# Kernel optimization log

Hardware: AMD Instinct MI355X
Metric: run time of the kernel (lower is better)

## Reference

```python
import jax, jax.numpy as jnp
import numpy as np

C = 64
SIZE = 448
PATCH = 14
P2 = PATCH * PATCH                 # 196, per-chunk token count
SPLIT = (SIZE * SIZE) // P2        # 1024 chunks
TG = PATCH * 4                     # 56, pooled global resolution
POOL = SIZE // TG                  # 8, exact avg-pool factor
EPS = 1e-5


def setup_inputs() -> dict:
    key = jax.random.key(0)
    ks = jax.random.split(key, 10)
    b = 2
    x = jax.random.normal(ks[0], (b, C, SIZE, SIZE), dtype=jnp.float32)
    s = 1.0 / np.sqrt(C)
    return {
        "x": x,
        "gn_w": jnp.ones((C,), jnp.float32),
        "gn_b": jnp.zeros((C,), jnp.float32),
        "q_w": jax.random.normal(ks[1], (C, C), jnp.float32) * s,
        "q_b": jnp.zeros((C,), jnp.float32),
        "k_w": jax.random.normal(ks[2], (C, C), jnp.float32) * s,
        "k_b": jnp.zeros((C,), jnp.float32),
        "v_w": jax.random.normal(ks[3], (C, C), jnp.float32) * s,
        "v_b": jnp.zeros((C,), jnp.float32),
        "proj_w": jax.random.normal(ks[4], (C, C), jnp.float32) * s,
    }


def _conv1x1(t, W, bias=None):
    out = jnp.einsum('oc,bchw->bohw', W, t)
    if bias is not None:
        out = out + bias[None, :, None, None]
    return out


def _group_norm(x, w, b):
    # GroupNorm(num_groups=1): normalize over (C,H,W) per sample
    mean = x.mean(axis=(1, 2, 3), keepdims=True)
    var = x.var(axis=(1, 2, 3), keepdims=True)
    xn = (x - mean) * jax.lax.rsqrt(var + EPS)
    return xn * w[None, :, None, None] + b[None, :, None, None]


def reference(x, gn_w, gn_b, q_w, q_b, k_w, k_b, v_w, v_b, proj_w):
    b, c, h, w = x.shape
    xn = _group_norm(x, gn_w, gn_b)
    q = _conv1x1(xn, q_w, q_b)
    k = _conv1x1(xn, k_w, k_b)
    v = _conv1x1(xn, v_w, v_b)

    # ---- patch-local attention (channels*chunks as feature dim S) ----
    S = c * SPLIT  # 65536
    qf = q.reshape(b, S, P2)
    kf = k.reshape(b, S, P2)
    vf = v.reshape(b, S, P2)
    wm = jnp.einsum('bsp,bsq->bpq', qf, kf) * (S ** -0.5)  # [b,196,196]
    wm = jax.nn.softmax(wm, axis=2)
    # h[b,s,q'] = sum_k v[b,s,k] * wm[b,q',k]
    hp = jnp.einsum('bsk,bqk->bsq', vf, wm).reshape(b, c, h, w)

    # ---- global pooled attention ----
    pool = lambda t: t.reshape(b, c, TG, POOL, TG, POOL).mean(axis=(3, 5))
    qg = pool(q).reshape(b, c, TG * TG)
    kg = pool(k).reshape(b, c, TG * TG)
    vg = pool(v).reshape(b, c, TG * TG)
    wg = jnp.einsum('bcp,bcq->bpq', qg, kg) * (c ** -0.5)  # [b,3136,3136]
    wg = jax.nn.softmax(wg, axis=2)
    hg = jnp.einsum('bck,bqk->bcq', vg, wg).reshape(b, c, TG, TG)
    hg = jnp.repeat(jnp.repeat(hg, POOL, axis=2), POOL, axis=3)

    h_in = 0.75 * hp + 0.25 * hg
    out = _conv1x1(h_in, proj_w)  # proj_out, no bias
    return x + out
```

## Files before the change

kernel.cpp:

```cpp
#include <hip/hip_runtime.h>

#define NB 2
#define NC 64
#define HW 200704
#define CHW 12845056
#define P2 196
#define NCHUNK 1024
#define NCELL 3136
#define WMN 38416

typedef __attribute__((ext_vector_type(8))) short bfrag;
typedef __attribute__((ext_vector_type(4))) float ffrag;
typedef __attribute__((ext_vector_type(4))) short short4v;
typedef __attribute__((ext_vector_type(4))) float float4v;

#define MFMA16(A,B,C) __builtin_amdgcn_mfma_f32_16x16x32_bf16(A,B,C,0,0,0)

__device__ __forceinline__ short f2bf(float f) {
  unsigned u = __builtin_bit_cast(unsigned, f);
  u = u + 0x7FFFu + ((u >> 16) & 1u);
  return (short)(u >> 16);
}

__global__ __launch_bounds__(64) void k1_stats_pool(
    const float* __restrict__ x, float* __restrict__ xpool, float* __restrict__ partials) {
  int bx = blockIdx.x;
  int batch = bx / (64*56);
  int c = (bx / 56) % 64;
  int pr = bx % 56;
  int l = threadIdx.x;
  const float* xp = x + (size_t)batch*CHW + (size_t)c*HW + pr*8*448;
  float cell = 0.f, s2 = 0.f;
  if (l < 56) {
    #pragma unroll
    for (int r = 0; r < 8; ++r) {
      float4v a = *(const float4v*)(xp + r*448 + l*8);
      float4v b = *(const float4v*)(xp + r*448 + l*8 + 4);
      #pragma unroll
      for (int j = 0; j < 4; ++j) { cell += a[j] + b[j]; s2 += a[j]*a[j] + b[j]*b[j]; }
    }
    xpool[((size_t)batch*64 + c)*NCELL + pr*56 + l] = cell * (1.f/64.f);
  }
  float s1 = (l < 56) ? cell : 0.f;
  #pragma unroll
  for (int m = 1; m < 64; m <<= 1) { s1 += __shfl_xor(s1, m, 64); s2 += __shfl_xor(s2, m, 64); }
  if (l == 0) { partials[bx*2] = s1; partials[bx*2 + 1] = s2; }
}

__global__ __launch_bounds__(256) void k1b_reduce(
    const float* __restrict__ partials, float* __restrict__ stats) {
  __shared__ float red[2][256];
  int t = threadIdx.x;
  for (int b = 0; b < NB; ++b) {
    float s1 = 0.f, s2 = 0.f;
    for (int i = t; i < 3584; i += 256) {
      s1 += partials[(b*3584 + i)*2];
      s2 += partials[(b*3584 + i)*2 + 1];
    }
    red[0][t] = s1; red[1][t] = s2;
    __syncthreads();
    for (int m = 128; m > 0; m >>= 1) {
      if (t < m) { red[0][t] += red[0][t+m]; red[1][t] += red[1][t+m]; }
      __syncthreads();
    }
    if (t == 0) { stats[b*2] = red[0][0]; stats[b*2+1] = red[1][0]; }
    __syncthreads();
  }
}

__global__ __launch_bounds__(256) void k2_qkv(
    const float* __restrict__ x, const float* __restrict__ gnw, const float* __restrict__ gnb,
    const float* __restrict__ qw, const float* __restrict__ qb,
    const float* __restrict__ kw, const float* __restrict__ kb,
    const float* __restrict__ vw, const float* __restrict__ vb,
    const float* __restrict__ stats,
    short* __restrict__ qx, short* __restrict__ kx, short* __restrict__ vnat) {
  __shared__ __attribute__((aligned(16))) short xnt[256*72];
  int bx = blockIdx.x;
  int batch = bx / 784;
  int px0 = (bx % 784) * 256;
  int t = threadIdx.x;
  float s1 = stats[batch*2], s2 = stats[batch*2+1];
  float mean = s1 * (1.f/CHW);
  float rstd = rsqrtf(s2*(1.f/CHW) - mean*mean + 1e-5f);
  for (int it = 0; it < 64; it += 4) {
    float vv[4];
    #pragma unroll
    for (int r = 0; r < 4; ++r) {
      float v = x[(size_t)batch*CHW + (size_t)(it+r)*HW + px0 + t];
      vv[r] = (v - mean) * rstd * gnw[it+r] + gnb[it+r];
    }
    short4v s;
    #pragma unroll
    for (int r = 0; r < 4; ++r) s[r] = f2bf(vv[r]);
    *(short4v*)(xnt + t*72 + it) = s;
  }
  __syncthreads();
  int l = t & 63, w = t >> 6, li = l & 15, q_ = l >> 4;
  bfrag bfr[4][2];
  #pragma unroll
  for (int nn = 0; nn < 4; ++nn) {
    int row = (w*4 + nn)*16 + li;
    bfr[nn][0] = *(const bfrag*)(xnt + row*72 + q_*8);
    bfr[nn][1] = *(const bfrag*)(xnt + row*72 + 32 + q_*8);
  }
  const float* Ws[3] = {qw, kw, vw};
  const float* Bs[3] = {qb, kb, vb};
  for (int T = 0; T < 3; ++T) {
    ffrag acc[4][4];
    #pragma unroll
    for (int mt = 0; mt < 4; ++mt) {
      bfrag a0, a1;
      const float* wp = Ws[T] + (mt*16 + li)*64;
      #pragma unroll
      for (int j = 0; j < 8; ++j) { a0[j] = f2bf(wp[q_*8 + j]); a1[j] = f2bf(wp[32 + q_*8 + j]); }
      #pragma unroll
      for (int nn = 0; nn < 4; ++nn) {
        ffrag z = {0.f,0.f,0.f,0.f};
        z = MFMA16(a0, bfr[nn][0], z);
        z = MFMA16(a1, bfr[nn][1], z);
        acc[mt][nn] = z;
      }
    }
    if (T < 2) {
      short* dstb = (T == 0 ? qx : kx) + (size_t)batch*HW*64;
      #pragma unroll
      for (int nn = 0; nn < 4; ++nn) {
        int px = px0 + (w*4 + nn)*16 + li;
        #pragma unroll
        for (int mt = 0; mt < 4; ++mt) {
          float4v bias = *(const float4v*)(Bs[T] + mt*16 + q_*4);
          short4v s;
          #pragma unroll
          for (int r = 0; r < 4; ++r) s[r] = f2bf(acc[mt][nn][r] + bias[r]);
          *(short4v*)(dstb + (size_t)px*64 + mt*16 + q_*4) = s;
        }
      }
    } else {
      #pragma unroll
      for (int nn = 0; nn < 4; ++nn) {
        int px = px0 + (w*4 + nn)*16 + li;
        #pragma unroll
        for (int mt = 0; mt < 4; ++mt) {
          float4v bias = *(const float4v*)(Bs[T] + mt*16 + q_*4);
          #pragma unroll
          for (int r = 0; r < 4; ++r) {
            int c = mt*16 + q_*4 + r;
            vnat[((size_t)batch*64 + c)*HW + px] = f2bf(acc[mt][nn][r] + bias[r]);
          }
        }
      }
    }
  }
}

__global__ __launch_bounds__(256) void k2a_pool_qkv(
    const float* __restrict__ xpool, const float* __restrict__ stats,
    const float* __restrict__ gnw, const float* __restrict__ gnb,
    const float* __restrict__ qw, const float* __restrict__ qb,
    const float* __restrict__ kw, const float* __restrict__ kb,
    const float* __restrict__ vw, const float* __restrict__ vb,
    short* __restrict__ qgt, short* __restrict__ kgt, short* __restrict__ vgn) {
  __shared__ float xs[64][64];
  int bx = blockIdx.x;
  int batch = bx / 49;
  int j0 = (bx % 49) * 64;
  int t = threadIdx.x;
  float s1 = stats[batch*2], s2 = stats[batch*2+1];
  float mean = s1 * (1.f/CHW);
  float rstd = rsqrtf(s2*(1.f/CHW) - mean*mean + 1e-5f);
  #pragma unroll
  for (int it = 0; it < 16; ++it) {
    int idx = t + it*256;
    int c = idx >> 6, jl = idx & 63;
    float v = xpool[((size_t)batch*64 + c)*NCELL + j0 + jl];
    xs[c][jl] = (v - mean)*rstd*gnw[c] + gnb[c];
  }
  __syncthreads();
  int jl = t & 63;
  int og = (t >> 6) * 16;
  int j = j0 + jl;
  for (int T = 0; T < 3; ++T) {
    const float* W  = (T==0 ? qw : (T==1 ? kw : vw));
    const float* Bv = (T==0 ? qb : (T==1 ? kb : vb));
    float o16[16];
    #pragma unroll
    for (int oo = 0; oo < 16; ++oo) o16[oo] = Bv[og+oo];
    for (int c = 0; c < 64; ++c) {
      float xv = xs[c][jl];
      #pragma unroll
      for (int oo = 0; oo < 16; ++oo) o16[oo] += W[(og+oo)*64 + c] * xv;
    }
    if (T < 2) {
      short* dst = (T==0 ? qgt : kgt) + ((size_t)batch*NCELL + j)*64 + og;
      #pragma unroll
      for (int oo = 0; oo < 16; oo += 4) {
        short4v s;
        #pragma unroll
        for (int r = 0; r < 4; ++r) s[r] = f2bf(o16[oo+r]);
        *(short4v*)(dst + oo) = s;
      }
    } else {
      #pragma unroll
      for (int oo = 0; oo < 16; ++oo)
        vgn[((size_t)batch*64 + og + oo)*NCELL + j] = f2bf(o16[oo]);
    }
  }
}

__global__ __launch_bounds__(512) void k3_wm(
    const short* __restrict__ qx, const short* __restrict__ kx, float* __restrict__ wmacc) {
  int bx = blockIdx.x;
  int batch = bx >> 6;
  int slab = bx & 63;
  int t = threadIdx.x;
  int l = t & 63, w = t >> 6, li = l & 15, q_ = l >> 4;
  int wm_ = w >> 2, wn = w & 3;
  int m0 = wm_ * 7, mcnt = wm_ ? 6 : 7;
  int nt0 = wn ? 4 + (wn-1)*3 : 0, ncnt = wn ? 3 : 4;
  ffrag acc[7][4];
  #pragma unroll
  for (int i = 0; i < 7; ++i)
    #pragma unroll
    for (int j = 0; j < 4; ++j) acc[i][j] = (ffrag){0.f,0.f,0.f,0.f};
  const short* qbase = qx + (size_t)batch*HW*64;
  const short* kbase = kx + (size_t)batch*HW*64;
  for (int c8 = 0; c8 < 16; ++c8) {
    int chunk = slab*16 + c8;
    const short* qc = qbase + (size_t)chunk*P2*64;
    const short* kc = kbase + (size_t)chunk*P2*64;
    #pragma unroll
    for (int ks = 0; ks < 2; ++ks) {
      int koff = ks*32 + q_*8;
      bfrag af[7], bf[4];
      #pragma unroll
      for (int mi = 0; mi < 7; ++mi) if (mi < mcnt)
        af[mi] = *(const bfrag*)(qc + (size_t)((m0+mi)*16 + li)*64 + koff);
      #pragma unroll
      for (int ni = 0; ni < 4; ++ni) if (ni < ncnt)
        bf[ni] = *(const bfrag*)(kc + (size_t)((nt0+ni)*16 + li)*64 + koff);
      #pragma unroll
      for (int mi = 0; mi < 7; ++mi) if (mi < mcnt)
        #pragma unroll
        for (int ni = 0; ni < 4; ++ni) if (ni < ncnt)
          acc[mi][ni] = MFMA16(af[mi], bf[ni], acc[mi][ni]);
    }
  }
  float* wdst = wmacc + (size_t)batch*WMN;
  #pragma unroll
  for (int mi = 0; mi < 7; ++mi) if (mi < mcnt)
    #pragma unroll
    for (int ni = 0; ni < 4; ++ni) if (ni < ncnt) {
      int qcol = (nt0+ni)*16 + li;
      if (qcol < 196)
        #pragma unroll
        for (int r = 0; r < 4; ++r) {
          int prow = (m0+mi)*16 + q_*4 + r;
          if (prow < 196) atomicAdd(wdst + prow*196 + qcol, acc[mi][ni][r]);
        }
    }
}

__global__ __launch_bounds__(64) void k4_softmax(
    const float* __restrict__ wmacc, short* __restrict__ P) {
  int bx = blockIdx.x;
  int batch = bx / 208;
  int p = bx % 208;
  int l = threadIdx.x;
  short* prow = P + ((size_t)batch*208 + p)*224;
  if (p >= 196) { for (int j = l; j < 224; j += 64) prow[j] = 0; return; }
  const float* src = wmacc + (size_t)batch*WMN + p*196;
  float v[4]; float mx = -1e30f;
  #pragma unroll
  for (int i = 0; i < 4; ++i) {
    int q = l + i*64;
    v[i] = (q < 196) ? src[q]*(1.f/256.f) : -1e30f;
    mx = fmaxf(mx, v[i]);
  }
  #pragma unroll
  for (int m = 1; m < 64; m <<= 1) mx = fmaxf(mx, __shfl_xor(mx, m, 64));
  float s = 0.f;
  #pragma unroll
  for (int i = 0; i < 4; ++i) { v[i] = __expf(v[i] - mx); s += v[i]; }
  #pragma unroll
  for (int m = 1; m < 64; m <<= 1) s += __shfl_xor(s, m, 64);
  float inv = 1.f / s;
  #pragma unroll
  for (int i = 0; i < 4; ++i) {
    int q = l + i*64;
    if (q < 224) prow[q] = (q < 196) ? f2bf(v[i]*inv) : (short)0;
  }
}

__global__ __launch_bounds__(256) void k5_gattn(
    const short* __restrict__ qgt, const short* __restrict__ kgt,
    const short* __restrict__ vgn, float* __restrict__ hgt) {
  __shared__ __attribute__((aligned(16))) short Pl[4][16][72];
  __shared__ __attribute__((aligned(16))) float alph[4][16];
  __shared__ __attribute__((aligned(16))) float lsum[4][16];
  int bx = blockIdx.x;
  int batch = bx / 49;
  int t = threadIdx.x;
  int w = t >> 6, l = t & 63, li = l & 15, q_ = l >> 4;
  int i0 = (bx % 49)*64 + w*16;
  const short* qg = qgt + (size_t)batch*NCELL*64;
  const short* kg = kgt + (size_t)batch*NCELL*64;
  const short* vg = vgn + (size_t)batch*64*NCELL;
  bfrag bq0 = *(const bfrag*)(qg + (size_t)(i0+li)*64 + q_*8);
  bfrag bq1 = *(const bfrag*)(qg + (size_t)(i0+li)*64 + 32 + q_*8);
  float m_run = -1e30f, l_run = 0.f;
  ffrag oa[4];
  #pragma unroll
  for (int i = 0; i < 4; ++i) oa[i] = (ffrag){0.f,0.f,0.f,0.f};
  for (int jt = 0; jt < 49; ++jt) {
    int j0 = jt*64;
    ffrag st[4];
    #pragma unroll
    for (int mt = 0; mt < 4; ++mt) {
      bfrag a0 = *(const bfrag*)(kg + (size_t)(j0 + mt*16 + li)*64 + q_*8);
      bfrag a1 = *(const bfrag*)(kg + (size_t)(j0 + mt*16 + li)*64 + 32 + q_*8);
      ffrag z = {0.f,0.f,0.f,0.f};
      z = MFMA16(a0, bq0, z);
      z = MFMA16(a1, bq1, z);
      st[mt] = z;
    }
    float mx = -1e30f;
    #pragma unroll
    for (int mt = 0; mt < 4; ++mt)
      #pragma unroll
      for (int r = 0; r < 4; ++r) { st[mt][r] *= 0.125f; mx = fmaxf(mx, st[mt][r]); }
    mx = fmaxf(mx, __shfl_xor(mx, 16, 64));
    mx = fmaxf(mx, __shfl_xor(mx, 32, 64));
    float m_new = fmaxf(m_run, mx);
    float alpha = __expf(m_run - m_new);
    float ps = 0.f;
    short4v pk[4];
    #pragma unroll
    for (int mt = 0; mt < 4; ++mt)
      #pragma unroll
      for (int r = 0; r < 4; ++r) { float e = __expf(st[mt][r] - m_new); ps += e; pk[mt][r] = f2bf(e); }
    ps += __shfl_xor(ps, 16, 64);
    ps += __shfl_xor(ps, 32, 64);
    l_run = l_run*alpha + ps;
    m_run = m_new;
    #pragma unroll
    for (int mt = 0; mt < 4; ++mt) *(short4v*)(&Pl[w][li][mt*16 + q_*4]) = pk[mt];
    alph[w][li] = alpha;
    __syncthreads();
    float4v al = *(const float4v*)(&alph[w][q_*4]);
    #pragma unroll
    for (int nt = 0; nt < 4; ++nt)
      #pragma unroll
      for (int r = 0; r < 4; ++r) oa[nt][r] *= al[r];
    #pragma unroll
    for (int ks = 0; ks < 2; ++ks) {
      bfrag a = *(const bfrag*)(&Pl[w][li][ks*32 + q_*8]);
      #pragma unroll
      for (int nt = 0; nt < 4; ++nt) {
        bfrag b = *(const bfrag*)(vg + (size_t)(nt*16 + li)*NCELL + j0 + ks*32 + q_*8);
        oa[nt] = MFMA16(a, b, oa[nt]);
      }
    }
    __syncthreads();
  }
  lsum[w][li] = l_run;
  __syncthreads();
  float4v lv = *(const float4v*)(&lsum[w][q_*4]);
  float* dst = hgt + (size_t)batch*NCELL*64;
  #pragma unroll
  for (int r = 0; r < 4; ++r) {
    float inv = 1.f / lv[r];
    int i = i0 + q_*4 + r;
    #pragma unroll
    for (int nt = 0; nt < 4; ++nt) dst[(size_t)i*64 + nt*16 + li] = oa[nt][r] * inv;
  }
}

__global__ __launch_bounds__(256) void k6_hp_proj(
    const short* __restrict__ vnat, const short* __restrict__ P,
    const float* __restrict__ hgt, const float* __restrict__ projw,
    const float* __restrict__ x, float* __restrict__ out) {
  __shared__ __attribute__((aligned(16))) short smem[208*72];
  short* vch = smem;
  short* hl  = smem;
  float* fs  = (float*)smem;
  int bx = blockIdx.x;
  int batch = bx >> 10;
  int chunk = bx & 1023;
  int t = threadIdx.x;
  const short* vsrc = vnat + (size_t)batch*64*HW + chunk*P2;
  for (int idx = t; idx < 3136; idx += 256) {
    int c = idx / 49, po = idx % 49;
    *(short4v*)(vch + c*232 + po*4) = *(const short4v*)(vsrc + (size_t)c*HW + po*4);
  }
  for (int idx = t; idx < 448; idx += 256) {
    int c = idx / 7, po = idx % 7;
    *(short4v*)(vch + c*232 + 196 + po*4) = (short4v){0,0,0,0};
  }
  __syncthreads();
  int l = t & 63, w = t >> 6, li = l & 15, q_ = l >> 4;
  int nt0 = w ? 4 + (w-1)*3 : 0;
  int ncnt = w ? 3 : 4;
  const short* Pb = P + (size_t)batch*208*224;
  ffrag acc[4][4];
  #pragma unroll
  for (int i = 0; i < 4; ++i)
    #pragma unroll
    for (int j = 0; j < 4; ++j) acc[i][j] = (ffrag){0.f,0.f,0.f,0.f};
  #pragma unroll
  for (int ks = 0; ks < 7; ++ks) {
    int koff = ks*32 + q_*8;
    bfrag av[4];
    #pragma unroll
    for (int mt = 0; mt < 4; ++mt) av[mt] = *(const bfrag*)(vch + (mt*16 + li)*232 + koff);
    #pragma unroll
    for (int ni = 0; ni < 4; ++ni) if (ni < ncnt) {
      bfrag bp = *(const bfrag*)(Pb + (size_t)((nt0+ni)*16 + li)*224 + koff);
      #pragma unroll
      for (int mt = 0; mt < 4; ++mt) acc[mt][ni] = MFMA16(av[mt], bp, acc[mt][ni]);
    }
  }
  __syncthreads();
  const float* hgb = hgt + (size_t)batch*NCELL*64;
  #pragma unroll
  for (int ni = 0; ni < 4; ++ni) if (ni < ncnt) {
    int pp = (nt0+ni)*16 + li;
    if (pp < 196) {
      int g = chunk*P2 + pp;
      int hh = g / 448, ww_ = g % 448;
      int cell = (hh >> 3)*56 + (ww_ >> 3);
      #pragma unroll
      for (int mt = 0; mt < 4; ++mt) {
        float4v hgv = *(const float4v*)(hgb + (size_t)cell*64 + mt*16 + q_*4);
        short4v s;
        #pragma unroll
        for (int r = 0; r < 4; ++r) s[r] = f2bf(0.75f*acc[mt][ni][r] + 0.25f*hgv[r]);
        *(short4v*)(hl + pp*72 + mt*16 + q_*4) = s;
      }
    }
  }
  for (int idx = t; idx < 216; idx += 256) {
    int rr = 196 + idx/18, cc = (idx%18)*4;
    *(short4v*)(hl + rr*72 + cc) = (short4v){0,0,0,0};
  }
  __syncthreads();
  ffrag acc2[4][4];
  #pragma unroll
  for (int i = 0; i < 4; ++i)
    #pragma unroll
    for (int j = 0; j < 4; ++j) acc2[i][j] = (ffrag){0.f,0.f,0.f,0.f};
  #pragma unroll
  for (int ks = 0; ks < 2; ++ks) {
    bfrag aw[4];
    #pragma unroll
    for (int mt = 0; mt < 4; ++mt) {
      const float* wp = projw + (mt*16 + li)*64 + ks*32 + q_*8;
      #pragma unroll
      for (int j = 0; j < 8; ++j) aw[mt][j] = f2bf(wp[j]);
    }
    #pragma unroll
    for (int ni = 0; ni < 4; ++ni) if (ni < ncnt) {
      bfrag bh = *(const bfrag*)(hl + ((nt0+ni)*16 + li)*72 + ks*32 + q_*8);
      #pragma unroll
      for (int mt = 0; mt < 4; ++mt) acc2[mt][ni] = MFMA16(aw[mt], bh, acc2[mt][ni]);
    }
  }
  __syncthreads();
  const float* xb = x + (size_t)batch*CHW;
  float* ob = out + (size_t)batch*CHW;
  #pragma unroll
  for (int h = 0; h < 2; ++h) {
    #pragma unroll
    for (int ni = 0; ni < 4; ++ni) if (ni < ncnt) {
      int pp = (nt0+ni)*16 + li;
      if (pp < 196) {
        #pragma unroll
        for (int mt = 0; mt < 2; ++mt) {
          #pragma unroll
          for (int r = 0; r < 4; ++r)
            fs[(mt*16 + q_*4 + r)*204 + pp] = acc2[h*2 + mt][ni][r];
        }
      }
    }
    __syncthreads();
    for (int idx = t; idx < 32*49; idx += 256) {
      int c = idx / 49, po = idx % 49;
      size_t off = (size_t)(h*32 + c)*HW + (size_t)chunk*P2 + po*4;
      float4v xv = *(const float4v*)(xb + off);
      float4v fv = *(const float4v*)(fs + c*204 + po*4);
      float4v o;
      #pragma unroll
      for (int r = 0; r < 4; ++r) o[r] = xv[r] + fv[r];
      *(float4v*)(ob + off) = o;
    }
    __syncthreads();
  }
}

extern "C" void kernel_launch(void* const* d_in, const int* in_sizes, int n_in,
                              void* d_out, int out_size, void* d_ws, size_t ws_size,
                              hipStream_t stream) {
  (void)in_sizes; (void)n_in; (void)out_size; (void)ws_size;
  const float* x   = (const float*)d_in[0];
  const float* gnw = (const float*)d_in[1];
  const float* gnb = (const float*)d_in[2];
  const float* qw  = (const float*)d_in[3];
  const float* qb  = (const float*)d_in[4];
  const float* kw  = (const float*)d_in[5];
  const float* kb  = (const float*)d_in[6];
  const float* vw  = (const float*)d_in[7];
  const float* vb  = (const float*)d_in[8];
  const float* pw  = (const float*)d_in[9];
  float* out = (float*)d_out;
  char* ws = (char*)d_ws;

  short* qx    = (short*)(ws + 0);
  short* kx    = (short*)(ws + 51380224);
  short* vnat  = (short*)(ws + 102760448);
  float* xpool = (float*)(ws + 154140672);
  short* qgt   = (short*)(ws + 155746304);
  short* kgt   = (short*)(ws + 156549120);
  short* vgn   = (short*)(ws + 157351936);
  float* hgt   = (float*)(ws + 158154752);
  short* P     = (short*)(ws + 159760384);
  float* wmacc = (float*)(ws + 159946752);
  float* stats = (float*)(ws + 160254080);
  float* partials = (float*)(ws + 159760384);

  hipMemsetAsync(ws + 159946752, 0, 307328, stream);
  k1_stats_pool<<<dim3(NB*64*56), dim3(64),  0, stream>>>(x, xpool, partials);
  k1b_reduce   <<<dim3(1),        dim3(256), 0, stream>>>(partials, stats);
  k2_qkv       <<<dim3(NB*784),   dim3(256), 0, stream>>>(x, gnw, gnb, qw, qb, kw, kb, vw, vb, stats, qx, kx, vnat);
  k2a_pool_qkv <<<dim3(NB*49),    dim3(256), 0, stream>>>(xpool, stats, gnw, gnb, qw, qb, kw, kb, vw, vb, qgt, kgt, vgn);
  k3_wm        <<<dim3(NB*64),    dim3(512), 0, stream>>>(qx, kx, wmacc);
  k4_softmax   <<<dim3(NB*208),   dim3(64),  0, stream>>>(wmacc, P);
  k5_gattn     <<<dim3(NB*49),    dim3(256), 0, stream>>>(qgt, kgt, vgn, hgt);
  k6_hp_proj   <<<dim3(NB*1024),  dim3(256), 0, stream>>>(vnat, P, hgt, pw, x, out);
}
```

Baseline: 682.3 us.

## Split global attention KV loop across waves with in-block softmax merge

The global pooled attention kernel now assigns 16 query rows per block and splits the 49 key tiles across the block's four waves, merging the partial (max, sum, output) states through shared memory at the end. This raises the grid from 98 to 392 blocks to fill more compute units, and it removes the per-iteration block barriers. In exchange, each wave reloads the same query fragment, and there is extra shared memory plus a final rescale-and-reduce step.

```diff
diff --git a/kernel.cpp b/kernel.cpp
--- a/kernel.cpp
+++ b/kernel.cpp
@@ -297,12 +297,13 @@
     const short* __restrict__ vgn, float* __restrict__ hgt) {
   __shared__ __attribute__((aligned(16))) short Pl[4][16][72];
   __shared__ __attribute__((aligned(16))) float alph[4][16];
-  __shared__ __attribute__((aligned(16))) float lsum[4][16];
-  int bx = blockIdx.x;
-  int batch = bx / 49;
+  __shared__ __attribute__((aligned(16))) float Om[4][16][64];
+  __shared__ __attribute__((aligned(16))) float ml[4][2][16];
+  int bx = blockIdx.x;
+  int batch = bx / 196;
+  int i0 = (bx % 196) * 16;
   int t = threadIdx.x;
   int w = t >> 6, l = t & 63, li = l & 15, q_ = l >> 4;
-  int i0 = (bx % 49)*64 + w*16;
   const short* qg = qgt + (size_t)batch*NCELL*64;
   const short* kg = kgt + (size_t)batch*NCELL*64;
   const short* vg = vgn + (size_t)batch*64*NCELL;
@@ -312,7 +313,7 @@
   ffrag oa[4];
   #pragma unroll
   for (int i = 0; i < 4; ++i) oa[i] = (ffrag){0.f,0.f,0.f,0.f};
-  for (int jt = 0; jt < 49; ++jt) {
+  for (int jt = w; jt < 49; jt += 4) {
     int j0 = jt*64;
     ffrag st[4];
     #pragma unroll
@@ -346,7 +347,6 @@
     #pragma unroll
     for (int mt = 0; mt < 4; ++mt) *(short4v*)(&Pl[w][li][mt*16 + q_*4]) = pk[mt];
     alph[w][li] = alpha;
-    __syncthreads();
     float4v al = *(const float4v*)(&alph[w][q_*4]);
     #pragma unroll
     for (int nt = 0; nt < 4; ++nt)
@@ -361,19 +361,34 @@
         oa[nt] = MFMA16(a, b, oa[nt]);
       }
     }
-    __syncthreads();
-  }
-  lsum[w][li] = l_run;
-  __syncthreads();
-  float4v lv = *(const float4v*)(&lsum[w][q_*4]);
-  float* dst = hgt + (size_t)batch*NCELL*64;
-  #pragma unroll
-  for (int r = 0; r < 4; ++r) {
-    float inv = 1.f / lv[r];
-    int i = i0 + q_*4 + r;
-    #pragma unroll
-    for (int nt = 0; nt < 4; ++nt) dst[(size_t)i*64 + nt*16 + li] = oa[nt][r] * inv;
-  }
+  }
+  ml[w][0][li] = m_run;
+  ml[w][1][li] = l_run;
+  #pragma unroll
+  for (int nt = 0; nt < 4; ++nt)
+    #pragma unroll
+    for (int r = 0; r < 4; ++r)
+      Om[w][q_*4 + r][nt*16 + li] = oa[nt][r];
+  __syncthreads();
+  int qq = t >> 4, c4 = (t & 15) * 4;
+  float m0 = ml[0][0][qq], m1 = ml[1][0][qq], m2 = ml[2][0][qq], m3 = ml[3][0][qq];
+  float ms = fmaxf(fmaxf(m0, m1), fmaxf(m2, m3));
+  float s0 = __expf(m0 - ms), s1 = __expf(m1 - ms);
+  float s2 = __expf(m2 - ms), s3 = __expf(m3 - ms);
+  float lt = ml[0][1][qq]*s0 + ml[1][1][qq]*s1 + ml[2][1][qq]*s2 + ml[3][1][qq]*s3;
+  float inv = 1.f / lt;
+  float sw[4] = {s0, s1, s2, s3};
+  float4v o = {0.f, 0.f, 0.f, 0.f};
+  #pragma unroll
+  for (int w2 = 0; w2 < 4; ++w2) {
+    float4v ov = *(const float4v*)(&Om[w2][qq][c4]);
+    #pragma unroll
+    for (int r = 0; r < 4; ++r) o[r] += ov[r] * sw[w2];
+  }
+  float4v outv;
+  #pragma unroll
+  for (int r = 0; r < 4; ++r) outv[r] = o[r] * inv;
+  *(float4v*)(hgt + (size_t)batch*NCELL*64 + (size_t)(i0 + qq)*64 + c4) = outv;
 }
 
 __global__ __launch_bounds__(256) void k6_hp_proj(
@@ -534,6 +549,6 @@
   k2a_pool_qkv <<<dim3(NB*49),    dim3(256), 0, stream>>>(xpool, stats, gnw, gnb, qw, qb, kw, kb, vw, vb, qgt, kgt, vgn);
   k3_wm        <<<dim3(NB*64),    dim3(512), 0, stream>>>(qx, kx, wmacc);
   k4_softmax   <<<dim3(NB*208),   dim3(64),  0, stream>>>(wmacc, P);
-  k5_gattn     <<<dim3(NB*49),    dim3(256), 0, stream>>>(qgt, kgt, vgn, hgt);
+  k5_gattn     <<<dim3(NB*196),   dim3(256), 0, stream>>>(qgt, kgt, vgn, hgt);
   k6_hp_proj   <<<dim3(NB*1024),  dim3(256), 0, stream>>>(vnat, P, hgt, pw, x, out);
 }
```

Result: faster. 603.8 us (-11.5%).
